# Optimization experiments

Measured on AMD Instinct MI355X. Metric: run time of the kernel, lower is better.

## Reference

```python
import jax, jax.numpy as jnp
import numpy as np
from jax.ops import segment_sum

N = 100000
E = 1600000
NFEAT = 512
NHID = 256
NCLASS = 64
K = 8
ALPHA = 0.1
NEG_SLOPE = 0.2


def setup_inputs() -> dict:
    key = jax.random.key(0)
    ks = jax.random.split(key, 16)
    x = jax.random.normal(ks[0], (N, NFEAT), dtype=jnp.float32)
    src = jax.random.randint(ks[1], (E,), 0, N)
    dst = jax.random.randint(ks[2], (E,), 0, N)
    weights = jax.random.uniform(ks[3], (E, 1), dtype=jnp.float32)
    latp = jax.random.normal(ks[4], (N, NCLASS), dtype=jnp.float32) * 0.1
    W_in = jax.random.normal(ks[5], (NFEAT, NHID), dtype=jnp.float32) * (1.0 / np.sqrt(NFEAT))
    W_out = jax.random.normal(ks[6], (NHID, NCLASS), dtype=jnp.float32) * (1.0 / np.sqrt(NHID))
    Ws1 = jax.random.normal(ks[7], (NCLASS, NCLASS), dtype=jnp.float32) * (1.0 / np.sqrt(NCLASS))
    b1 = jnp.zeros((NCLASS,), dtype=jnp.float32)
    Ws2 = jax.random.normal(ks[8], (NCLASS, NCLASS), dtype=jnp.float32) * (1.0 / np.sqrt(NCLASS))
    b2 = jnp.zeros((NCLASS,), dtype=jnp.float32)
    attn_l = jax.random.normal(ks[9], (1, NCLASS), dtype=jnp.float32) * 0.1
    attn_r = jax.random.normal(ks[10], (1, NCLASS), dtype=jnp.float32) * 0.1
    s_attn = jax.random.normal(ks[11], (1, NCLASS), dtype=jnp.float32) * 0.1
    beta = jnp.zeros((1, 1), dtype=jnp.float32)
    theta = jnp.zeros((1, 1), dtype=jnp.float32)
    aw = jax.random.normal(ks[12], (1, 2), dtype=jnp.float32) * 0.1
    return {"x": x, "src": src, "dst": dst, "weights": weights, "latp": latp,
            "W_in": W_in, "W_out": W_out, "Ws1": Ws1, "b1": b1, "Ws2": Ws2, "b2": b2,
            "attn_l": attn_l, "attn_r": attn_r, "s_attn": s_attn,
            "beta": beta, "theta": theta, "aw": aw}


def reference(x, src, dst, weights, latp, W_in, W_out, Ws1, b1, Ws2, b2,
              attn_l, attn_r, s_attn, beta, theta, aw):
    # node MLP (dropout is identity in eval mode)
    h = jax.nn.elu(x @ W_in) @ W_out                      # [N, nclass]
    # position MLP on latp
    hl = jax.nn.elu(latp @ Ws1 + b1)
    hl = jax.nn.elu(hl @ Ws2 + b2)                        # [N, nclass]

    # edge attention scores
    lr = jax.nn.leaky_relu(h, NEG_SLOPE)
    el = jnp.sum(lr * attn_l, axis=-1)                    # [N]
    er = jnp.sum(lr * attn_r, axis=-1)                    # [N]
    e = el[src] + er[dst]                                 # [E]
    se = jnp.sum((hl * s_attn)[src] * hl[dst], axis=-1)   # [E]
    e = e + se

    # divergence terms
    sdf = jnp.sum((h[src] - h[dst]) ** 2, axis=-1)        # [E]
    sds = jnp.sum((hl[src] - hl[dst]) ** 2, axis=-1)      # [E]
    wt = jax.nn.softmax(aw, axis=1)
    d = wt[0, 0] * sdf + wt[0, 1] * sds

    betaw = 2.0 / (jnp.exp(-beta[0, 0]) + 1.0)
    ew = jnp.exp(e - betaw * d) + 1e-9                    # [E]

    # symmetric ('both') edge-weight normalization
    deg_src = segment_sum(ew, src, num_segments=N)        # out-degree weight sums
    deg_dst = segment_sum(ew, dst, num_segments=N)        # in-degree weight sums
    w = (deg_src ** -0.5)[src] * (deg_dst ** -0.5)[dst] * ew
    perm = 1e-9 / (jnp.exp(-theta[0, 0]) + 1.0)           # WL perturbation
    w = w + perm                                          # [E]

    # k-step weighted propagation
    feat0 = h
    fp = h
    wcol = w[:, None]
    for _ in range(K):
        agg = segment_sum(fp[src] * wcol, dst, num_segments=N)
        fp = (1.0 - ALPHA) * agg + ALPHA * feat0

    # position loss
    lp_loss = jnp.sum(hl[src] * weights * hl[dst])

    out = jax.nn.log_softmax(jax.nn.elu(fp), axis=1)
    return out, lp_loss
```

## Files before the change

kernel.cpp:

```cpp
#include <hip/hip_runtime.h>
#include <math.h>

#define NN 100000
#define EE 1600000
#define NFEATC 512
#define NHIDC 256
#define NCC 64
#define ALPHA_C 0.1f
#define NSLOPE_C 0.2f
#define SCAN_NB ((NN + 255) / 256)

typedef __attribute__((ext_vector_type(8))) short short8;
typedef __attribute__((ext_vector_type(4))) short short4v;
typedef __attribute__((ext_vector_type(4))) float floatx4;

__device__ __forceinline__ short f2bf(float f) {
    unsigned u = __float_as_uint(f);
    unsigned r = (u + 0x7FFFu + ((u >> 16) & 1u)) >> 16;
    return (short)r;
}
__device__ __forceinline__ float bf2f(short s) {
    return __uint_as_float(((unsigned)(unsigned short)s) << 16);
}

__global__ __launch_bounds__(256)
void castWT_kernel(const float* __restrict__ W, short* __restrict__ WT, int K, int Ncols)
{
    int k = blockIdx.x;
    int n = threadIdx.x;
    if (k < K && n < Ncols)
        WT[(size_t)n * K + k] = f2bf(W[(size_t)k * Ncols + n]);
}

__global__ __launch_bounds__(256)
void cast_bf_kernel(const float* __restrict__ in, short* __restrict__ out, int n4)
{
    int i = blockIdx.x * 256 + threadIdx.x;
    if (i >= n4) return;
    float4 v = reinterpret_cast<const float4*>(in)[i];
    short4v o;
    o[0] = f2bf(v.x); o[1] = f2bf(v.y); o[2] = f2bf(v.z); o[3] = f2bf(v.w);
    reinterpret_cast<short4v*>(out)[i] = o;
}

__global__ __launch_bounds__(256)
void gemm1_mfma_kernel(const float* __restrict__ x, const short* __restrict__ WT,
                       float* __restrict__ h1, int M)
{
    __shared__ short As[128][40];
    __shared__ short Bs[256][40];
    const int tid = threadIdx.x;
    const int bm = blockIdx.x * 128;
    const int wave = tid >> 6;
    const int lane = tid & 63;
    const int wm = wave >> 1;
    const int wn = wave & 1;
    const int l16 = lane & 15;
    const int quad = lane >> 4;

    floatx4 acc[4][8];
    #pragma unroll
    for (int i = 0; i < 4; ++i)
        #pragma unroll
        for (int j = 0; j < 8; ++j)
            acc[i][j] = (floatx4){0.f, 0.f, 0.f, 0.f};

    const int ar = tid >> 1;
    const int ah = tid & 1;
    const int xrow = bm + ar;
    const float* xp = x + (size_t)xrow * NFEATC + ah * 16;
    const short* wp = WT + (size_t)tid * NFEATC;

    for (int kt = 0; kt < NFEATC; kt += 32) {
        float4 a0, a1, a2, a3;
        if (xrow < M) {
            a0 = *reinterpret_cast<const float4*>(xp + kt + 0);
            a1 = *reinterpret_cast<const float4*>(xp + kt + 4);
            a2 = *reinterpret_cast<const float4*>(xp + kt + 8);
            a3 = *reinterpret_cast<const float4*>(xp + kt + 12);
        } else {
            a0 = a1 = a2 = a3 = make_float4(0.f, 0.f, 0.f, 0.f);
        }
        const short8* wq = reinterpret_cast<const short8*>(wp + kt);
        short8 b0 = wq[0], b1 = wq[1], b2 = wq[2], b3 = wq[3];

        short8 s0, s1;
        s0[0] = f2bf(a0.x); s0[1] = f2bf(a0.y); s0[2] = f2bf(a0.z); s0[3] = f2bf(a0.w);
        s0[4] = f2bf(a1.x); s0[5] = f2bf(a1.y); s0[6] = f2bf(a1.z); s0[7] = f2bf(a1.w);
        s1[0] = f2bf(a2.x); s1[1] = f2bf(a2.y); s1[2] = f2bf(a2.z); s1[3] = f2bf(a2.w);
        s1[4] = f2bf(a3.x); s1[5] = f2bf(a3.y); s1[6] = f2bf(a3.z); s1[7] = f2bf(a3.w);

        __syncthreads();
        *reinterpret_cast<short8*>(&As[ar][ah * 16 + 0]) = s0;
        *reinterpret_cast<short8*>(&As[ar][ah * 16 + 8]) = s1;
        *reinterpret_cast<short8*>(&Bs[tid][0])  = b0;
        *reinterpret_cast<short8*>(&Bs[tid][8])  = b1;
        *reinterpret_cast<short8*>(&Bs[tid][16]) = b2;
        *reinterpret_cast<short8*>(&Bs[tid][24]) = b3;
        __syncthreads();

        short8 af[4], bfr[8];
        #pragma unroll
        for (int mi = 0; mi < 4; ++mi)
            af[mi] = *reinterpret_cast<const short8*>(&As[wm * 64 + mi * 16 + l16][quad * 8]);
        #pragma unroll
        for (int ni = 0; ni < 8; ++ni)
            bfr[ni] = *reinterpret_cast<const short8*>(&Bs[wn * 128 + ni * 16 + l16][quad * 8]);
        #pragma unroll
        for (int mi = 0; mi < 4; ++mi)
            #pragma unroll
            for (int ni = 0; ni < 8; ++ni)
                acc[mi][ni] = __builtin_amdgcn_mfma_f32_16x16x32_bf16(af[mi], bfr[ni], acc[mi][ni], 0, 0, 0);
    }

    #pragma unroll
    for (int mi = 0; mi < 4; ++mi) {
        #pragma unroll
        for (int r = 0; r < 4; ++r) {
            int row = bm + wm * 64 + mi * 16 + quad * 4 + r;
            if (row >= M) continue;
            float* outp = h1 + (size_t)row * NHIDC + wn * 128 + l16;
            #pragma unroll
            for (int ni = 0; ni < 8; ++ni) {
                float v = acc[mi][ni][r];
                v = (v > 0.f) ? v : (expf(v) - 1.f);
                outp[ni * 16] = v;
            }
        }
    }
}

template<int ACT>
__global__ __launch_bounds__(256)
void gemm_kernel(const float* __restrict__ A, const float* __restrict__ B,
                 const float* __restrict__ bias, float* __restrict__ C,
                 int M, int K, int Ncols)
{
    __shared__ float As[16][68];
    __shared__ float Bs[16][64];
    const int tid = threadIdx.x;
    const int bm = blockIdx.x * 64;
    const int bn = blockIdx.y * 64;
    const int m0 = (tid & 15) * 4;
    const int n0 = (tid >> 4) * 4;
    float acc[4][4] = {};

    const int am = bm + (tid >> 2);
    const int ak = (tid & 3) * 4;
    const int bk = tid >> 4;
    const int bn4 = bn + (tid & 15) * 4;

    for (int kt = 0; kt < K; kt += 16) {
        float4 av;
        if (am < M) av = *reinterpret_cast<const float4*>(A + (size_t)am * K + kt + ak);
        else        av = make_float4(0.f, 0.f, 0.f, 0.f);
        float4 bv = *reinterpret_cast<const float4*>(B + (size_t)(kt + bk) * Ncols + bn4);
        __syncthreads();
        As[ak + 0][tid >> 2] = av.x;
        As[ak + 1][tid >> 2] = av.y;
        As[ak + 2][tid >> 2] = av.z;
        As[ak + 3][tid >> 2] = av.w;
        *reinterpret_cast<float4*>(&Bs[bk][(tid & 15) * 4]) = bv;
        __syncthreads();
        #pragma unroll
        for (int k = 0; k < 16; ++k) {
            float4 a4 = *reinterpret_cast<const float4*>(&As[k][m0]);
            float4 b4 = *reinterpret_cast<const float4*>(&Bs[k][n0]);
            float a_[4] = {a4.x, a4.y, a4.z, a4.w};
            float b_[4] = {b4.x, b4.y, b4.z, b4.w};
            #pragma unroll
            for (int i = 0; i < 4; ++i)
                #pragma unroll
                for (int j = 0; j < 4; ++j)
                    acc[i][j] = fmaf(a_[i], b_[j], acc[i][j]);
        }
    }

    float bvals[4] = {0.f, 0.f, 0.f, 0.f};
    if (bias) {
        bvals[0] = bias[bn + n0 + 0]; bvals[1] = bias[bn + n0 + 1];
        bvals[2] = bias[bn + n0 + 2]; bvals[3] = bias[bn + n0 + 3];
    }
    #pragma unroll
    for (int i = 0; i < 4; ++i) {
        int r = bm + m0 + i;
        if (r >= M) break;
        float v[4];
        #pragma unroll
        for (int j = 0; j < 4; ++j) {
            float t = acc[i][j] + bvals[j];
            if (ACT == 1) t = (t > 0.f) ? t : (expf(t) - 1.f);
            v[j] = t;
        }
        float4 o = make_float4(v[0], v[1], v[2], v[3]);
        *reinterpret_cast<float4*>(C + (size_t)r * Ncols + bn + n0) = o;
    }
}

__global__ __launch_bounds__(256)
void attn_kernel(const float* __restrict__ h, const float* __restrict__ attn_l,
                 const float* __restrict__ attn_r, float* __restrict__ el, float* __restrict__ er)
{
    int node = blockIdx.x * 4 + (threadIdx.x >> 6);
    int lane = threadIdx.x & 63;
    if (node >= NN) return;
    float v = h[(size_t)node * 64 + lane];
    float lr = (v > 0.f) ? v : NSLOPE_C * v;
    float a = lr * attn_l[lane];
    float b = lr * attn_r[lane];
    #pragma unroll
    for (int m = 1; m < 64; m <<= 1) {
        a += __shfl_xor(a, m);
        b += __shfl_xor(b, m);
    }
    if (lane == 0) { el[node] = a; er[node] = b; }
}

__global__ __launch_bounds__(256)
void count_kernel(const int* __restrict__ dst, int* __restrict__ cnt)
{
    int e = blockIdx.x * 256 + threadIdx.x;
    if (e < EE) atomicAdd(cnt + dst[e], 1);
}

__global__ __launch_bounds__(256)
void scan1_kernel(const int* __restrict__ cnt, int* __restrict__ partials)
{
    int i = blockIdx.x * 256 + threadIdx.x;
    int v = (i < NN) ? cnt[i] : 0;
    #pragma unroll
    for (int m = 1; m < 64; m <<= 1) v += __shfl_xor(v, m);
    __shared__ int sred[4];
    if ((threadIdx.x & 63) == 0) sred[threadIdx.x >> 6] = v;
    __syncthreads();
    if (threadIdx.x == 0)
        partials[blockIdx.x] = sred[0] + sred[1] + sred[2] + sred[3];
}

__global__ __launch_bounds__(512)
void scan2_kernel(int* __restrict__ partials)
{
    __shared__ int s[512];
    int t = threadIdx.x;
    int v = (t < SCAN_NB) ? partials[t] : 0;
    s[t] = v;
    __syncthreads();
    #pragma unroll
    for (int off = 1; off < 512; off <<= 1) {
        int add = (t >= off) ? s[t - off] : 0;
        __syncthreads();
        s[t] += add;
        __syncthreads();
    }
    if (t < SCAN_NB) partials[t] = s[t] - v;
}

__global__ __launch_bounds__(256)
void scan3_kernel(const int* __restrict__ cnt, const int* __restrict__ partials,
                  int* __restrict__ row, int* __restrict__ cur)
{
    __shared__ int s[256];
    int t = threadIdx.x;
    int i = blockIdx.x * 256 + t;
    int v = (i < NN) ? cnt[i] : 0;
    s[t] = v;
    __syncthreads();
    #pragma unroll
    for (int off = 1; off < 256; off <<= 1) {
        int add = (t >= off) ? s[t - off] : 0;
        __syncthreads();
        s[t] += add;
        __syncthreads();
    }
    int r = partials[blockIdx.x] + s[t] - v;
    if (i < NN) { row[i] = r; cur[i] = r; }
    if (i == NN - 1) row[NN] = r + v;
}

__global__ __launch_bounds__(256)
void bucket_kernel(const int* __restrict__ src, const int* __restrict__ dst,
                   const float* __restrict__ wts, int* __restrict__ cur,
                   int* __restrict__ csr_src, float* __restrict__ csr_wts)
{
    int e = blockIdx.x * 256 + threadIdx.x;
    if (e >= EE) return;
    int d = dst[e];
    int pos = atomicAdd(cur + d, 1);
    csr_src[pos] = src[e];
    csr_wts[pos] = wts[e];
}

__global__ __launch_bounds__(256)
void edge2_kernel(const int* __restrict__ row, const int* __restrict__ csr_src,
                  const float* __restrict__ csr_wts,
                  const float* __restrict__ h, const float* __restrict__ hl,
                  const float* __restrict__ el, const float* __restrict__ er,
                  const float* __restrict__ s_attn, const float* __restrict__ beta,
                  const float* __restrict__ aw,
                  float* __restrict__ ew, float* __restrict__ deg_s,
                  float* __restrict__ deg_d, float* __restrict__ lp_part)
{
    int node = blockIdx.x * 4 + (threadIdx.x >> 6);
    int lane = threadIdx.x & 63;
    int sub = lane >> 4;
    int f = lane & 15;
    float lp_p = 0.f;
    if (node < NN) {
        int b = row[node], en = row[node + 1];
        const float4 hd = *reinterpret_cast<const float4*>(h  + (size_t)node * 64 + f * 4);
        const float4 ld = *reinterpret_cast<const float4*>(hl + (size_t)node * 64 + f * 4);
        const float4 sa = *reinterpret_cast<const float4*>(s_attn + f * 4);
        float erd = er[node];
        float betaw = 2.f / (expf(-beta[0]) + 1.f);
        float a0 = aw[0], a1 = aw[1];
        float mxw = fmaxf(a0, a1);
        float e0 = expf(a0 - mxw), e1 = expf(a1 - mxw);
        float inv = 1.f / (e0 + e1);
        float w0 = e0 * inv, w1 = e1 * inv;
        float degd = 0.f;
        for (int e = b + sub; e < en; e += 4) {
            int s = csr_src[e];
            const float4 hs = *reinterpret_cast<const float4*>(h  + (size_t)s * 64 + f * 4);
            const float4 ls = *reinterpret_cast<const float4*>(hl + (size_t)s * 64 + f * 4);
            float se_p  = ls.x * sa.x * ld.x + ls.y * sa.y * ld.y
                        + ls.z * sa.z * ld.z + ls.w * sa.w * ld.w;
            float dot_p = ls.x * ld.x + ls.y * ld.y + ls.z * ld.z + ls.w * ld.w;
            float dx = hs.x - hd.x, dy = hs.y - hd.y, dz = hs.z - hd.z, dw = hs.w - hd.w;
            float sdf_p = dx * dx + dy * dy + dz * dz + dw * dw;
            float ex = ls.x - ld.x, ey = ls.y - ld.y, ez = ls.z - ld.z, ec = ls.w - ld.w;
            float sds_p = ex * ex + ey * ey + ez * ez + ec * ec;
            #pragma unroll
            for (int m = 1; m < 16; m <<= 1) {
                se_p  += __shfl_xor(se_p, m);
                dot_p += __shfl_xor(dot_p, m);
                sdf_p += __shfl_xor(sdf_p, m);
                sds_p += __shfl_xor(sds_p, m);
            }
            if (f == 0) {
                float evv = el[s] + erd + se_p;
                float dd = w0 * sdf_p + w1 * sds_p;
                float v = expf(evv - betaw * dd) + 1e-9f;
                ew[e] = v;
                atomicAdd(deg_s + s, v);
                degd += v;
                lp_p += dot_p * csr_wts[e];
            }
        }
        #pragma unroll
        for (int m = 16; m < 64; m <<= 1) degd += __shfl_xor(degd, m);
        if (lane == 0) deg_d[node] = degd;
    }
    #pragma unroll
    for (int m = 16; m < 64; m <<= 1) lp_p += __shfl_xor(lp_p, m);
    __shared__ float lred[4];
    if ((threadIdx.x & 63) == 0) lred[threadIdx.x >> 6] = lp_p;
    __syncthreads();
    if (threadIdx.x == 0) lp_part[blockIdx.x] = lred[0] + lred[1] + lred[2] + lred[3];
}

__global__ __launch_bounds__(256)
void reduce_kernel(const float* __restrict__ part, int n, float* __restrict__ out)
{
    float s = 0.f;
    for (int i = threadIdx.x; i < n; i += 256) s += part[i];
    #pragma unroll
    for (int m = 1; m < 64; m <<= 1) s += __shfl_xor(s, m);
    __shared__ float sd[4];
    if ((threadIdx.x & 63) == 0) sd[threadIdx.x >> 6] = s;
    __syncthreads();
    if (threadIdx.x == 0) out[0] = sd[0] + sd[1] + sd[2] + sd[3];
}

__global__ __launch_bounds__(256)
void wnorm_csr_kernel(const int* __restrict__ row, const int* __restrict__ csr_src,
                      const float* __restrict__ ew, const float* __restrict__ deg_s,
                      const float* __restrict__ deg_d, const float* __restrict__ theta,
                      float* __restrict__ csr_w)
{
    int node = blockIdx.x * 16 + (threadIdx.x >> 4);
    int f = threadIdx.x & 15;
    if (node >= NN) return;
    int b = row[node], en = row[node + 1];
    float perm = 1e-9f / (expf(-theta[0]) + 1.f);
    float dr = rsqrtf(deg_d[node]);
    for (int e = b + f; e < en; e += 16) {
        float v = ew[e] * rsqrtf(deg_s[csr_src[e]]) * dr + perm;
        csr_w[e] = (1.0f - ALPHA_C) * v;
    }
}

template<int FINAL>
__global__ __launch_bounds__(256)
void prop_kernel(const short* __restrict__ fin, const float* __restrict__ h,
                 const int* __restrict__ row, const int* __restrict__ csr_src,
                 const float* __restrict__ csr_w,
                 short* __restrict__ foutb, float* __restrict__ outf)
{
    int node = blockIdx.x * 4 + (threadIdx.x >> 6);
    int lane = threadIdx.x & 63;
    int sub = lane >> 3;
    int f = lane & 7;
    if (node >= NN) return;
    int b = row[node], en = row[node + 1];
    float acc[8] = {};
    for (int e = b + sub; e < en; e += 8) {
        int s = csr_src[e];
        float wv = csr_w[e];
        short8 v = *reinterpret_cast<const short8*>(fin + (size_t)s * 64 + f * 8);
        #pragma unroll
        for (int i = 0; i < 8; ++i)
            acc[i] = fmaf(wv, bf2f(v[i]), acc[i]);
    }
    #pragma unroll
    for (int m = 8; m < 64; m <<= 1)
        #pragma unroll
        for (int i = 0; i < 8; ++i)
            acc[i] += __shfl_xor(acc[i], m);
    if (sub == 0) {
        const float4 h0 = *reinterpret_cast<const float4*>(h + (size_t)node * 64 + f * 8 + 0);
        const float4 h1v = *reinterpret_cast<const float4*>(h + (size_t)node * 64 + f * 8 + 4);
        float o[8];
        o[0] = fmaf(ALPHA_C, h0.x, acc[0]);
        o[1] = fmaf(ALPHA_C, h0.y, acc[1]);
        o[2] = fmaf(ALPHA_C, h0.z, acc[2]);
        o[3] = fmaf(ALPHA_C, h0.w, acc[3]);
        o[4] = fmaf(ALPHA_C, h1v.x, acc[4]);
        o[5] = fmaf(ALPHA_C, h1v.y, acc[5]);
        o[6] = fmaf(ALPHA_C, h1v.z, acc[6]);
        o[7] = fmaf(ALPHA_C, h1v.w, acc[7]);
        if (!FINAL) {
            short8 ob;
            #pragma unroll
            for (int i = 0; i < 8; ++i) ob[i] = f2bf(o[i]);
            *reinterpret_cast<short8*>(foutb + (size_t)node * 64 + f * 8) = ob;
        } else {
            float ev[8];
            #pragma unroll
            for (int i = 0; i < 8; ++i)
                ev[i] = (o[i] > 0.f) ? o[i] : (expf(o[i]) - 1.f);
            float mx = ev[0];
            #pragma unroll
            for (int i = 1; i < 8; ++i) mx = fmaxf(mx, ev[i]);
            #pragma unroll
            for (int m = 1; m < 8; m <<= 1) mx = fmaxf(mx, __shfl_xor(mx, m));
            float s = 0.f;
            #pragma unroll
            for (int i = 0; i < 8; ++i) s += expf(ev[i] - mx);
            #pragma unroll
            for (int m = 1; m < 8; m <<= 1) s += __shfl_xor(s, m);
            float ls = mx + logf(s);
            float4 o0 = make_float4(ev[0] - ls, ev[1] - ls, ev[2] - ls, ev[3] - ls);
            float4 o1 = make_float4(ev[4] - ls, ev[5] - ls, ev[6] - ls, ev[7] - ls);
            *reinterpret_cast<float4*>(outf + (size_t)node * 64 + f * 8 + 0) = o0;
            *reinterpret_cast<float4*>(outf + (size_t)node * 64 + f * 8 + 4) = o1;
        }
    }
}

extern "C" void kernel_launch(void* const* d_in, const int* in_sizes, int n_in,
                              void* d_out, int out_size, void* d_ws, size_t ws_size,
                              hipStream_t stream)
{
    const float* x      = (const float*)d_in[0];
    const int*   src    = (const int*)d_in[1];
    const int*   dst    = (const int*)d_in[2];
    const float* wts    = (const float*)d_in[3];
    const float* latp   = (const float*)d_in[4];
    const float* W_in   = (const float*)d_in[5];
    const float* W_out  = (const float*)d_in[6];
    const float* Ws1    = (const float*)d_in[7];
    const float* b1     = (const float*)d_in[8];
    const float* Ws2    = (const float*)d_in[9];
    const float* b2     = (const float*)d_in[10];
    const float* attn_l = (const float*)d_in[11];
    const float* attn_r = (const float*)d_in[12];
    const float* s_attn = (const float*)d_in[13];
    const float* beta   = (const float*)d_in[14];
    const float* theta  = (const float*)d_in[15];
    const float* aw     = (const float*)d_in[16];

    float* out = (float*)d_out;
    float* lp  = out + (size_t)NN * 64;

    char* w8 = (char*)d_ws;
    size_t off = 0;
    auto alloc = [&](size_t bytes) -> char* {
        char* p = w8 + off;
        off += (bytes + 255) / 256 * 256;
        return p;
    };
    float* big     = (float*)alloc((size_t)NN * 256 * 4);
    float* h1      = big;
    float* hl_tmp  = big;
    short* h_bf    = (short*)big;
    short* fpA_bf  = (short*)big + (size_t)NN * 64;
    short* fpB_bf  = (short*)big + (size_t)NN * 64 * 2;
    float* csr_wts = (float*)((short*)big + (size_t)NN * 64 * 3);
    float* h      = (float*)alloc((size_t)NN * 64 * 4);
    float* hl     = (float*)alloc((size_t)NN * 64 * 4);
    float* ew     = (float*)alloc((size_t)EE * 4);
    float* el     = (float*)alloc((size_t)NN * 4);
    float* er     = (float*)alloc((size_t)NN * 4);
    float* deg_s  = (float*)alloc((size_t)NN * 4);
    float* deg_d  = (float*)alloc((size_t)NN * 4);
    int*   cnt    = (int*)alloc((size_t)NN * 4);
    int*   row    = (int*)alloc((size_t)(NN + 1) * 4);
    int*   cur    = (int*)alloc((size_t)NN * 4);
    int*   csr_src= (int*)alloc((size_t)EE * 4);
    float* csr_w  = (float*)alloc((size_t)EE * 4);
    float* lp_part= (float*)alloc((size_t)100000 * 4);
    int*   partials=(int*)alloc((size_t)SCAN_NB * 4);
    short* WT     = (short*)alloc((size_t)NHIDC * NFEATC * 2);

    hipMemsetAsync(cnt,   0, (size_t)NN * 4, stream);
    hipMemsetAsync(deg_s, 0, (size_t)NN * 4, stream);

    const int MB = (NN + 63) / 64;

    castWT_kernel<<<NFEATC, 256, 0, stream>>>(W_in, WT, NFEATC, NHIDC);
    gemm1_mfma_kernel<<<(NN + 127) / 128, 256, 0, stream>>>(x, WT, h1, NN);

    gemm_kernel<0><<<dim3(MB, 1), 256, 0, stream>>>(h1, W_out, nullptr, h, NN, NHIDC, NCC);
    gemm_kernel<1><<<dim3(MB, 1), 256, 0, stream>>>(latp, Ws1, b1, hl_tmp, NN, NCC, NCC);
    gemm_kernel<1><<<dim3(MB, 1), 256, 0, stream>>>(hl_tmp, Ws2, b2, hl, NN, NCC, NCC);

    attn_kernel<<<NN / 4, 256, 0, stream>>>(h, attn_l, attn_r, el, er);
    count_kernel<<<EE / 256, 256, 0, stream>>>(dst, cnt);
    scan1_kernel<<<SCAN_NB, 256, 0, stream>>>(cnt, partials);
    scan2_kernel<<<1, 512, 0, stream>>>(partials);
    scan3_kernel<<<SCAN_NB, 256, 0, stream>>>(cnt, partials, row, cur);
    bucket_kernel<<<EE / 256, 256, 0, stream>>>(src, dst, wts, cur, csr_src, csr_wts);

    edge2_kernel<<<NN / 4, 256, 0, stream>>>(row, csr_src, csr_wts, h, hl, el, er,
                                             s_attn, beta, aw, ew, deg_s, deg_d, lp_part);
    reduce_kernel<<<1, 256, 0, stream>>>(lp_part, NN / 4, lp);

    wnorm_csr_kernel<<<NN / 16, 256, 0, stream>>>(row, csr_src, ew, deg_s, deg_d, theta, csr_w);

    cast_bf_kernel<<<(NN * 64 / 4 + 255) / 256, 256, 0, stream>>>(h, h_bf, NN * 64 / 4);

    const short* fin = h_bf;
    short* bufs[2] = {fpA_bf, fpB_bf};
    for (int it = 0; it < 7; ++it) {
        short* fo = bufs[it & 1];
        prop_kernel<0><<<NN / 4, 256, 0, stream>>>(fin, h, row, csr_src, csr_w, fo, nullptr);
        fin = fo;
    }
    prop_kernel<1><<<NN / 4, 256, 0, stream>>>(fin, h, row, csr_src, csr_w, nullptr, out);
}
```

Baseline: 1.322 ms.

## Expand squared-distance terms into per-node norms and unroll edge gathers by two

The attention kernel now also computes per-node squared norms of h and hl and folds them, scaled by the divergence weights, into per-node A/B scalars. The edge kernel then computes one fused dot product per edge instead of four separate reductions. Both the edge kernel and the propagation kernel are unrolled to process two edges per iteration, raising memory-level parallelism on the gathers. Expanding the squared differences can lose fp32 precision through cancellation when the inputs are near each other.

```diff
diff --git a/kernel.cpp b/kernel.cpp
--- a/kernel.cpp
+++ b/kernel.cpp
@@ -198,22 +198,38 @@
 }
 
 __global__ __launch_bounds__(256)
-void attn_kernel(const float* __restrict__ h, const float* __restrict__ attn_l,
-                 const float* __restrict__ attn_r, float* __restrict__ el, float* __restrict__ er)
+void attn2_kernel(const float* __restrict__ h, const float* __restrict__ hl,
+                  const float* __restrict__ attn_l, const float* __restrict__ attn_r,
+                  const float* __restrict__ beta, const float* __restrict__ aw,
+                  float* __restrict__ A, float* __restrict__ B)
 {
     int node = blockIdx.x * 4 + (threadIdx.x >> 6);
     int lane = threadIdx.x & 63;
     if (node >= NN) return;
     float v = h[(size_t)node * 64 + lane];
+    float u = hl[(size_t)node * 64 + lane];
     float lr = (v > 0.f) ? v : NSLOPE_C * v;
     float a = lr * attn_l[lane];
     float b = lr * attn_r[lane];
+    float nh = v * v;
+    float nl = u * u;
     #pragma unroll
     for (int m = 1; m < 64; m <<= 1) {
         a += __shfl_xor(a, m);
         b += __shfl_xor(b, m);
-    }
-    if (lane == 0) { el[node] = a; er[node] = b; }
+        nh += __shfl_xor(nh, m);
+        nl += __shfl_xor(nl, m);
+    }
+    if (lane == 0) {
+        float betaw = 2.f / (expf(-beta[0]) + 1.f);
+        float a0 = aw[0], a1 = aw[1];
+        float mxw = fmaxf(a0, a1);
+        float e0 = expf(a0 - mxw), e1 = expf(a1 - mxw);
+        float inv = 1.f / (e0 + e1);
+        float t = betaw * (e0 * inv * nh + e1 * inv * nl);
+        A[node] = a - t;
+        B[node] = b - t;
+    }
 }
 
 __global__ __launch_bounds__(256)
@@ -294,7 +310,7 @@
 void edge2_kernel(const int* __restrict__ row, const int* __restrict__ csr_src,
                   const float* __restrict__ csr_wts,
                   const float* __restrict__ h, const float* __restrict__ hl,
-                  const float* __restrict__ el, const float* __restrict__ er,
+                  const float* __restrict__ A, const float* __restrict__ B,
                   const float* __restrict__ s_attn, const float* __restrict__ beta,
                   const float* __restrict__ aw,
                   float* __restrict__ ew, float* __restrict__ deg_s,
@@ -307,43 +323,72 @@
     float lp_p = 0.f;
     if (node < NN) {
         int b = row[node], en = row[node + 1];
-        const float4 hd = *reinterpret_cast<const float4*>(h  + (size_t)node * 64 + f * 4);
-        const float4 ld = *reinterpret_cast<const float4*>(hl + (size_t)node * 64 + f * 4);
-        const float4 sa = *reinterpret_cast<const float4*>(s_attn + f * 4);
-        float erd = er[node];
         float betaw = 2.f / (expf(-beta[0]) + 1.f);
         float a0 = aw[0], a1 = aw[1];
         float mxw = fmaxf(a0, a1);
         float e0 = expf(a0 - mxw), e1 = expf(a1 - mxw);
         float inv = 1.f / (e0 + e1);
-        float w0 = e0 * inv, w1 = e1 * inv;
+        float c0 = 2.f * betaw * e0 * inv;
+        float c1 = 2.f * betaw * e1 * inv;
+        const float4 hd = *reinterpret_cast<const float4*>(h  + (size_t)node * 64 + f * 4);
+        const float4 ld = *reinterpret_cast<const float4*>(hl + (size_t)node * 64 + f * 4);
+        const float4 sa = *reinterpret_cast<const float4*>(s_attn + f * 4);
+        float4 P = make_float4(c0 * hd.x, c0 * hd.y, c0 * hd.z, c0 * hd.w);
+        float4 Q = make_float4(sa.x * ld.x, sa.y * ld.y, sa.z * ld.z, sa.w * ld.w);
+        float Bd = B[node];
         float degd = 0.f;
-        for (int e = b + sub; e < en; e += 4) {
-            int s = csr_src[e];
-            const float4 hs = *reinterpret_cast<const float4*>(h  + (size_t)s * 64 + f * 4);
-            const float4 ls = *reinterpret_cast<const float4*>(hl + (size_t)s * 64 + f * 4);
-            float se_p  = ls.x * sa.x * ld.x + ls.y * sa.y * ld.y
-                        + ls.z * sa.z * ld.z + ls.w * sa.w * ld.w;
-            float dot_p = ls.x * ld.x + ls.y * ld.y + ls.z * ld.z + ls.w * ld.w;
-            float dx = hs.x - hd.x, dy = hs.y - hd.y, dz = hs.z - hd.z, dw = hs.w - hd.w;
-            float sdf_p = dx * dx + dy * dy + dz * dz + dw * dw;
-            float ex = ls.x - ld.x, ey = ls.y - ld.y, ez = ls.z - ld.z, ec = ls.w - ld.w;
-            float sds_p = ex * ex + ey * ey + ez * ez + ec * ec;
+        int e = b + sub;
+        for (; e + 4 < en; e += 8) {
+            int s1 = csr_src[e];
+            int s2 = csr_src[e + 4];
+            const float4 hs1 = *reinterpret_cast<const float4*>(h  + (size_t)s1 * 64 + f * 4);
+            const float4 ls1 = *reinterpret_cast<const float4*>(hl + (size_t)s1 * 64 + f * 4);
+            const float4 hs2 = *reinterpret_cast<const float4*>(h  + (size_t)s2 * 64 + f * 4);
+            const float4 ls2 = *reinterpret_cast<const float4*>(hl + (size_t)s2 * 64 + f * 4);
+            float r1 = hs1.x * P.x + hs1.y * P.y + hs1.z * P.z + hs1.w * P.w
+                     + ls1.x * Q.x + ls1.y * Q.y + ls1.z * Q.z + ls1.w * Q.w;
+            float d31 = ls1.x * ld.x + ls1.y * ld.y + ls1.z * ld.z + ls1.w * ld.w;
+            float r2 = hs2.x * P.x + hs2.y * P.y + hs2.z * P.z + hs2.w * P.w
+                     + ls2.x * Q.x + ls2.y * Q.y + ls2.z * Q.z + ls2.w * Q.w;
+            float d32 = ls2.x * ld.x + ls2.y * ld.y + ls2.z * ld.z + ls2.w * ld.w;
             #pragma unroll
             for (int m = 1; m < 16; m <<= 1) {
-                se_p  += __shfl_xor(se_p, m);
-                dot_p += __shfl_xor(dot_p, m);
-                sdf_p += __shfl_xor(sdf_p, m);
-                sds_p += __shfl_xor(sds_p, m);
+                r1  += __shfl_xor(r1, m);
+                d31 += __shfl_xor(d31, m);
+                r2  += __shfl_xor(r2, m);
+                d32 += __shfl_xor(d32, m);
             }
             if (f == 0) {
-                float evv = el[s] + erd + se_p;
-                float dd = w0 * sdf_p + w1 * sds_p;
-                float v = expf(evv - betaw * dd) + 1e-9f;
-                ew[e] = v;
-                atomicAdd(deg_s + s, v);
-                degd += v;
-                lp_p += dot_p * csr_wts[e];
+                float v1 = expf(A[s1] + Bd + r1 + c1 * d31) + 1e-9f;
+                ew[e] = v1;
+                atomicAdd(deg_s + s1, v1);
+                degd += v1;
+                lp_p += d31 * csr_wts[e];
+                float v2 = expf(A[s2] + Bd + r2 + c1 * d32) + 1e-9f;
+                ew[e + 4] = v2;
+                atomicAdd(deg_s + s2, v2);
+                degd += v2;
+                lp_p += d32 * csr_wts[e + 4];
+            }
+        }
+        if (e < en) {
+            int s1 = csr_src[e];
+            const float4 hs1 = *reinterpret_cast<const float4*>(h  + (size_t)s1 * 64 + f * 4);
+            const float4 ls1 = *reinterpret_cast<const float4*>(hl + (size_t)s1 * 64 + f * 4);
+            float r1 = hs1.x * P.x + hs1.y * P.y + hs1.z * P.z + hs1.w * P.w
+                     + ls1.x * Q.x + ls1.y * Q.y + ls1.z * Q.z + ls1.w * Q.w;
+            float d31 = ls1.x * ld.x + ls1.y * ld.y + ls1.z * ld.z + ls1.w * ld.w;
+            #pragma unroll
+            for (int m = 1; m < 16; m <<= 1) {
+                r1  += __shfl_xor(r1, m);
+                d31 += __shfl_xor(d31, m);
+            }
+            if (f == 0) {
+                float v1 = expf(A[s1] + Bd + r1 + c1 * d31) + 1e-9f;
+                ew[e] = v1;
+                atomicAdd(deg_s + s1, v1);
+                degd += v1;
+                lp_p += d31 * csr_wts[e];
             }
         }
         #pragma unroll
@@ -403,13 +448,28 @@
     if (node >= NN) return;
     int b = row[node], en = row[node + 1];
     float acc[8] = {};
-    for (int e = b + sub; e < en; e += 8) {
-        int s = csr_src[e];
-        float wv = csr_w[e];
-        short8 v = *reinterpret_cast<const short8*>(fin + (size_t)s * 64 + f * 8);
+    int e = b + sub;
+    for (; e + 8 < en; e += 16) {
+        int s1 = csr_src[e];
+        float w1 = csr_w[e];
+        int s2 = csr_src[e + 8];
+        float w2 = csr_w[e + 8];
+        short8 v1 = *reinterpret_cast<const short8*>(fin + (size_t)s1 * 64 + f * 8);
+        short8 v2 = *reinterpret_cast<const short8*>(fin + (size_t)s2 * 64 + f * 8);
         #pragma unroll
         for (int i = 0; i < 8; ++i)
-            acc[i] = fmaf(wv, bf2f(v[i]), acc[i]);
+            acc[i] = fmaf(w1, bf2f(v1[i]), acc[i]);
+        #pragma unroll
+        for (int i = 0; i < 8; ++i)
+            acc[i] = fmaf(w2, bf2f(v2[i]), acc[i]);
+    }
+    if (e < en) {
+        int s1 = csr_src[e];
+        float w1 = csr_w[e];
+        short8 v1 = *reinterpret_cast<const short8*>(fin + (size_t)s1 * 64 + f * 8);
+        #pragma unroll
+        for (int i = 0; i < 8; ++i)
+            acc[i] = fmaf(w1, bf2f(v1[i]), acc[i]);
     }
     #pragma unroll
     for (int m = 8; m < 64; m <<= 1)
@@ -499,8 +559,8 @@
     float* h      = (float*)alloc((size_t)NN * 64 * 4);
     float* hl     = (float*)alloc((size_t)NN * 64 * 4);
     float* ew     = (float*)alloc((size_t)EE * 4);
-    float* el     = (float*)alloc((size_t)NN * 4);
-    float* er     = (float*)alloc((size_t)NN * 4);
+    float* Aarr   = (float*)alloc((size_t)NN * 4);
+    float* Barr   = (float*)alloc((size_t)NN * 4);
     float* deg_s  = (float*)alloc((size_t)NN * 4);
     float* deg_d  = (float*)alloc((size_t)NN * 4);
     int*   cnt    = (int*)alloc((size_t)NN * 4);
@@ -524,14 +584,14 @@
     gemm_kernel<1><<<dim3(MB, 1), 256, 0, stream>>>(latp, Ws1, b1, hl_tmp, NN, NCC, NCC);
     gemm_kernel<1><<<dim3(MB, 1), 256, 0, stream>>>(hl_tmp, Ws2, b2, hl, NN, NCC, NCC);
 
-    attn_kernel<<<NN / 4, 256, 0, stream>>>(h, attn_l, attn_r, el, er);
+    attn2_kernel<<<NN / 4, 256, 0, stream>>>(h, hl, attn_l, attn_r, beta, aw, Aarr, Barr);
     count_kernel<<<EE / 256, 256, 0, stream>>>(dst, cnt);
     scan1_kernel<<<SCAN_NB, 256, 0, stream>>>(cnt, partials);
     scan2_kernel<<<1, 512, 0, stream>>>(partials);
     scan3_kernel<<<SCAN_NB, 256, 0, stream>>>(cnt, partials, row, cur);
     bucket_kernel<<<EE / 256, 256, 0, stream>>>(src, dst, wts, cur, csr_src, csr_wts);
 
-    edge2_kernel<<<NN / 4, 256, 0, stream>>>(row, csr_src, csr_wts, h, hl, el, er,
+    edge2_kernel<<<NN / 4, 256, 0, stream>>>(row, csr_src, csr_wts, h, hl, Aarr, Barr,
                                              s_attn, beta, aw, ew, deg_s, deg_d, lp_part);
     reduce_kernel<<<1, 256, 0, stream>>>(lp_part, NN / 4, lp);
 
```

Measured after the change: 1.257 ms. 1.05x faster.
